# Performance work log

Measured on AMD Instinct MI355X. Metric: run time of the kernel, lower is better.

The kernel has to match this reference:

```python
import jax, jax.numpy as jnp
import numpy as np

B, N, DIN, DH, DOUT, E = 262144, 8, 3, 32, 1, 32


def setup_inputs() -> dict:
    key = jax.random.key(0)
    ks = jax.random.split(key, 8)
    x = jax.random.normal(ks[0], (B, N, DIN), dtype=jnp.float32)
    edge_index = jax.random.randint(ks[1], (2, E), 0, N, dtype=jnp.int64)
    s = lambda k, sh: jax.random.normal(k, sh, dtype=jnp.float32) * 0.1
    return {
        "x": x,
        "edge_index": edge_index,
        "W1": s(ks[2], (DIN, DH)),
        "b1": jnp.zeros((DH,), jnp.float32),
        "W2": s(ks[3], (DH, DH)),
        "b2": jnp.zeros((DH,), jnp.float32),
        "Wout": s(ks[4], (DH, DOUT)),
        "bout": jnp.zeros((DOUT,), jnp.float32),
    }


def _gcn_norm(edge_index, n):
    # add self loops, symmetric GCN normalization D^-1/2 (A+I) D^-1/2
    loops = jnp.arange(n, dtype=edge_index.dtype)
    src = jnp.concatenate([edge_index[0], loops])
    dst = jnp.concatenate([edge_index[1], loops])
    deg = jnp.zeros((n,), jnp.float32).at[dst].add(1.0)
    dinv = jax.lax.rsqrt(jnp.maximum(deg, 1e-12))
    norm = dinv[src] * dinv[dst]  # [E+N]
    return src, dst, norm


def _gcn_layer(h, W, b, src, dst, norm):
    hw = h @ W                              # [B, N, H]
    msg = hw[:, src, :] * norm[None, :, None]
    agg = jnp.zeros_like(hw).at[:, dst, :].add(msg)
    return agg + b


def reference(x, edge_index, W1, b1, W2, b2, Wout, bout):
    n = x.shape[1]
    src, dst, norm = _gcn_norm(edge_index, n)
    h = jax.nn.relu(_gcn_layer(x, W1, b1, src, dst, norm))
    h = jax.nn.relu(_gcn_layer(h, W2, b2, src, dst, norm))
    h = jax.nn.relu(h @ Wout + bout)        # [B, N, DOUT]
    # global_mean_pool with all-zero batch ids == mean over nodes
    return jnp.mean(h, axis=1)              # [B, DOUT]
```

## Files before the change

### kernel.cpp

```cpp
#include <hip/hip_runtime.h>


typedef __bf16 bf16x8 __attribute__((ext_vector_type(8)));
typedef float  f32x16 __attribute__((ext_vector_type(16)));

#define GPT 32

__global__ __launch_bounds__(256, 2) void gnn_kernel(
    const float* __restrict__ x,
    const int* __restrict__ ei,
    const float* __restrict__ W1,
    const float* __restrict__ b1,
    const float* __restrict__ W2,
    const float* __restrict__ b2,
    const float* __restrict__ Wout,
    const float* __restrict__ bout,
    float* __restrict__ out,
    int B, int ntiles)
{
    __shared__ float As[64];
    __shared__ float degs[8], dinvs[8];
    __shared__ float W1s[96], b1s[32], W2s[1024], b2s[32], Wouts[32];
    __shared__ float xs[2][GPT * 24];

    const int tid = threadIdx.x;

    if (tid < 96) W1s[tid] = W1[tid];
    if (tid < 64) As[tid] = 0.0f;
    if (tid < 32) { b1s[tid] = b1[tid]; b2s[tid] = b2[tid]; Wouts[tid] = Wout[tid]; }
    if (tid < 8)  degs[tid] = 1.0f;
    for (int i = tid; i < 1024; i += 256) W2s[i] = W2[i];
    __syncthreads();
    if (tid < 32) { int d = ei[32 + tid]; atomicAdd(&degs[d], 1.0f); }
    __syncthreads();
    if (tid < 8) dinvs[tid] = 1.0f / sqrtf(degs[tid]);
    __syncthreads();
    if (tid < 32) {
        int s = ei[tid], d = ei[32 + tid];
        atomicAdd(&As[d * 8 + s], dinvs[s] * dinvs[d]);
    } else if (tid < 40) {
        int n = tid - 32;
        atomicAdd(&As[n * 8 + n], dinvs[n] * dinvs[n]);
    }
    __syncthreads();

    const int lane = tid & 63;
    const int wv   = tid >> 6;
    const int r    = lane & 31;
    const int q    = lane >> 5;
    const int n8   = r & 7;
    const int gl   = r >> 3;
    const int g0   = wv * 4 + gl;
    const int g1   = 16 + wv * 4 + gl;

    float arow[8];
    #pragma unroll
    for (int m = 0; m < 8; m++) arow[m] = As[n8 * 8 + m];

    bf16x8 w1Ahi, w1Alo;
    #pragma unroll
    for (int j = 0; j < 8; j++) { w1Ahi[j] = (__bf16)0.0f; w1Alo[j] = (__bf16)0.0f; }
    #pragma unroll
    for (int j = 0; j < 3; j++) {
        float v = W1s[j * 32 + r];
        __bf16 h = (__bf16)v;
        w1Ahi[j] = h; w1Alo[j] = (__bf16)(v - (float)h);
    }
    {
        float v = b1s[r];
        __bf16 h = (__bf16)v;
        w1Ahi[3] = h; w1Alo[3] = (__bf16)(v - (float)h);
    }

    bf16x8 w2hi[2];
    #pragma unroll
    for (int s = 0; s < 2; s++) {
        #pragma unroll
        for (int j = 0; j < 8; j++) {
            int kk = 8 * s + j;
            int hid = (kk & 3) + 8 * (kk >> 2) + 4 * q;
            w2hi[s][j] = (__bf16)W2s[hid * 32 + r];
        }
    }
    bf16x8 a32hi[2];
    #pragma unroll
    for (int s = 0; s < 2; s++) {
        #pragma unroll
        for (int j = 0; j < 8; j++) {
            int kk = 8 * s + j;
            float v = ((kk >> 2) == gl) ? arow[(kk & 3) + 4 * q] : 0.0f;
            a32hi[s][j] = (__bf16)v;
        }
    }
    f32x16 zerov, b2rv;
    float woutr[16];
    #pragma unroll
    for (int k = 0; k < 16; k++) {
        int hk = (k & 3) + 8 * (k >> 2) + 4 * q;
        zerov[k] = 0.0f;
        b2rv[k] = b2s[hk];
        woutr[k] = Wouts[hk];
    }
    const float boutv = bout[0];

    const float4* x4 = reinterpret_cast<const float4*>(x);
    float4 nxt;
    if (tid < 192 && blockIdx.x < ntiles)
        nxt = x4[(long long)blockIdx.x * 192 + tid];
    int buf = 0;

    for (int tile = blockIdx.x; tile < ntiles; tile += gridDim.x) {
        const long long gbase = (long long)tile * GPT;
        if (tid < 192) *reinterpret_cast<float4*>(&xs[buf][tid * 4]) = nxt;
        __syncthreads();
        int tnext = tile + gridDim.x;
        if (tid < 192 && tnext < ntiles)
            nxt = x4[(long long)tnext * 192 + tid];

        float y00 = 0.f, y01 = 0.f, y02 = 0.f;
        {
            float xv[24];
            #pragma unroll
            for (int i = 0; i < 6; i++) {
                float4 v = *reinterpret_cast<float4*>(&xs[buf][g0 * 24 + i * 4]);
                xv[4 * i] = v.x; xv[4 * i + 1] = v.y; xv[4 * i + 2] = v.z; xv[4 * i + 3] = v.w;
            }
            #pragma unroll
            for (int m = 0; m < 8; m++) {
                y00 = fmaf(arow[m], xv[m * 3 + 0], y00);
                y01 = fmaf(arow[m], xv[m * 3 + 1], y01);
                y02 = fmaf(arow[m], xv[m * 3 + 2], y02);
            }
        }
        float y10 = 0.f, y11 = 0.f, y12 = 0.f;
        {
            float xv[24];
            #pragma unroll
            for (int i = 0; i < 6; i++) {
                float4 v = *reinterpret_cast<float4*>(&xs[buf][g1 * 24 + i * 4]);
                xv[4 * i] = v.x; xv[4 * i + 1] = v.y; xv[4 * i + 2] = v.z; xv[4 * i + 3] = v.w;
            }
            #pragma unroll
            for (int m = 0; m < 8; m++) {
                y10 = fmaf(arow[m], xv[m * 3 + 0], y10);
                y11 = fmaf(arow[m], xv[m * 3 + 1], y11);
                y12 = fmaf(arow[m], xv[m * 3 + 2], y12);
            }
        }

        bf16x8 yB0, yB1;
        #pragma unroll
        for (int j = 0; j < 8; j++) { yB0[j] = (__bf16)0.0f; yB1[j] = (__bf16)0.0f; }
        {
            __bf16 h0 = (__bf16)y00, h1 = (__bf16)y01, h2 = (__bf16)y02;
            yB0[0] = q ? (__bf16)(y00 - (float)h0) : h0;
            yB0[1] = q ? (__bf16)(y01 - (float)h1) : h1;
            yB0[2] = q ? (__bf16)(y02 - (float)h2) : h2;
            yB0[3] = q ? (__bf16)0.0f : (__bf16)1.0f;
            __bf16 g0h = (__bf16)y10, g1h = (__bf16)y11, g2h = (__bf16)y12;
            yB1[0] = q ? (__bf16)(y10 - (float)g0h) : g0h;
            yB1[1] = q ? (__bf16)(y11 - (float)g1h) : g1h;
            yB1[2] = q ? (__bf16)(y12 - (float)g2h) : g2h;
            yB1[3] = q ? (__bf16)0.0f : (__bf16)1.0f;
        }

        f32x16 vacc0, vacc1;
        vacc0 = __builtin_amdgcn_mfma_f32_32x32x16_bf16(w1Ahi, yB0, zerov, 0, 0, 0);
        vacc1 = __builtin_amdgcn_mfma_f32_32x32x16_bf16(w1Ahi, yB1, zerov, 0, 0, 0);
        vacc0 = __builtin_amdgcn_mfma_f32_32x32x16_bf16(w1Alo, yB0, vacc0, 0, 0, 0);
        vacc1 = __builtin_amdgcn_mfma_f32_32x32x16_bf16(w1Alo, yB1, vacc1, 0, 0, 0);

        bf16x8 phi0[2], phi1[2];
        #pragma unroll
        for (int s = 0; s < 2; s++) {
            #pragma unroll
            for (int j = 0; j < 8; j++) {
                phi0[s][j] = (__bf16)fmaxf(vacc0[8 * s + j], 0.0f);
                phi1[s][j] = (__bf16)fmaxf(vacc1[8 * s + j], 0.0f);
            }
        }

        vacc0 = __builtin_amdgcn_mfma_f32_32x32x16_bf16(phi0[0], w2hi[0], zerov, 0, 0, 0);
        vacc1 = __builtin_amdgcn_mfma_f32_32x32x16_bf16(phi1[0], w2hi[0], zerov, 0, 0, 0);
        vacc0 = __builtin_amdgcn_mfma_f32_32x32x16_bf16(phi0[1], w2hi[1], vacc0, 0, 0, 0);
        vacc1 = __builtin_amdgcn_mfma_f32_32x32x16_bf16(phi1[1], w2hi[1], vacc1, 0, 0, 0);

        bf16x8 thi0[2], thi1[2];
        #pragma unroll
        for (int s = 0; s < 2; s++) {
            #pragma unroll
            for (int j = 0; j < 8; j++) {
                thi0[s][j] = (__bf16)vacc0[8 * s + j];
                thi1[s][j] = (__bf16)vacc1[8 * s + j];
            }
        }

        vacc0 = __builtin_amdgcn_mfma_f32_32x32x16_bf16(thi0[0], a32hi[0], b2rv, 0, 0, 0);
        vacc1 = __builtin_amdgcn_mfma_f32_32x32x16_bf16(thi1[0], a32hi[0], b2rv, 0, 0, 0);
        vacc0 = __builtin_amdgcn_mfma_f32_32x32x16_bf16(thi0[1], a32hi[1], vacc0, 0, 0, 0);
        vacc1 = __builtin_amdgcn_mfma_f32_32x32x16_bf16(thi1[1], a32hi[1], vacc1, 0, 0, 0);

        float ss0 = 0.0f, ss1 = 0.0f;
        #pragma unroll
        for (int k = 0; k < 16; k++) {
            ss0 = fmaf(fmaxf(vacc0[k], 0.0f), woutr[k], ss0);
            ss1 = fmaf(fmaxf(vacc1[k], 0.0f), woutr[k], ss1);
        }
        ss0 += __shfl_xor(ss0, 32, 64);
        ss1 += __shfl_xor(ss1, 32, 64);
        float o0 = fmaxf(ss0 + boutv, 0.0f);
        float o1 = fmaxf(ss1 + boutv, 0.0f);
        o0 += __shfl_xor(o0, 1, 64);  o1 += __shfl_xor(o1, 1, 64);
        o0 += __shfl_xor(o0, 2, 64);  o1 += __shfl_xor(o1, 2, 64);
        o0 += __shfl_xor(o0, 4, 64);  o1 += __shfl_xor(o1, 4, 64);
        if (q == 0 && n8 == 0) {
            long long gg0 = gbase + g0;
            if (gg0 < (long long)B) out[gg0] = o0 * 0.125f;
            long long gg1 = gbase + g1;
            if (gg1 < (long long)B) out[gg1] = o1 * 0.125f;
        }
        buf ^= 1;
    }
}

extern "C" void kernel_launch(void* const* d_in, const int* in_sizes, int n_in,
                              void* d_out, int out_size, void* d_ws, size_t ws_size,
                              hipStream_t stream) {
    const float* x    = (const float*)d_in[0];
    const int*   ei   = (const int*)d_in[1];
    const float* W1   = (const float*)d_in[2];
    const float* b1   = (const float*)d_in[3];
    const float* W2   = (const float*)d_in[4];
    const float* b2   = (const float*)d_in[5];
    const float* Wout = (const float*)d_in[6];
    const float* bout = (const float*)d_in[7];
    float* out = (float*)d_out;
    (void)d_ws; (void)ws_size; (void)out_size; (void)n_in;

    const int B = in_sizes[0] / 24;
    const int ntiles = (B + GPT - 1) / GPT;
    const int grid = ntiles < 2048 ? ntiles : 2048;
    gnn_kernel<<<grid, 256, 0, stream>>>(x, ei, W1, b1, W2, b2, Wout, bout, out, B, ntiles);
}
```

Measured before the change: 32.34 us.

## Load each block's four tiles of x upfront instead of grid-stride double buffering

```diff
diff --git a/kernel.cpp b/kernel.cpp
--- a/kernel.cpp
+++ b/kernel.cpp
@@ -5,6 +5,7 @@
 typedef float  f32x16 __attribute__((ext_vector_type(16)));
 
 #define GPT 32
+#define TPB 4
 
 __global__ __launch_bounds__(256, 2) void gnn_kernel(
     const float* __restrict__ x,
@@ -16,12 +17,12 @@
     const float* __restrict__ Wout,
     const float* __restrict__ bout,
     float* __restrict__ out,
-    int B, int ntiles)
+    int B)
 {
     __shared__ float As[64];
     __shared__ float degs[8], dinvs[8];
     __shared__ float W1s[96], b1s[32], W2s[1024], b2s[32], Wouts[32];
-    __shared__ float xs[2][GPT * 24];
+    __shared__ float xs[TPB * GPT * 24];
 
     const int tid = threadIdx.x;
 
@@ -30,6 +31,14 @@
     if (tid < 32) { b1s[tid] = b1[tid]; b2s[tid] = b2[tid]; Wouts[tid] = Wout[tid]; }
     if (tid < 8)  degs[tid] = 1.0f;
     for (int i = tid; i < 1024; i += 256) W2s[i] = W2[i];
+    {
+        const float4* x4 = reinterpret_cast<const float4*>(x);
+        long long base4 = (long long)blockIdx.x * (TPB * GPT * 6);
+        float4* xs4 = reinterpret_cast<float4*>(xs);
+        #pragma unroll
+        for (int i = 0; i < 3; i++)
+            xs4[tid + 256 * i] = x4[base4 + tid + 256 * i];
+    }
     __syncthreads();
     if (tid < 32) { int d = ei[32 + tid]; atomicAdd(&degs[d], 1.0f); }
     __syncthreads();
@@ -103,26 +112,17 @@
     }
     const float boutv = bout[0];
 
-    const float4* x4 = reinterpret_cast<const float4*>(x);
-    float4 nxt;
-    if (tid < 192 && blockIdx.x < ntiles)
-        nxt = x4[(long long)blockIdx.x * 192 + tid];
-    int buf = 0;
-
-    for (int tile = blockIdx.x; tile < ntiles; tile += gridDim.x) {
-        const long long gbase = (long long)tile * GPT;
-        if (tid < 192) *reinterpret_cast<float4*>(&xs[buf][tid * 4]) = nxt;
-        __syncthreads();
-        int tnext = tile + gridDim.x;
-        if (tid < 192 && tnext < ntiles)
-            nxt = x4[(long long)tnext * 192 + tid];
+    #pragma unroll
+    for (int it = 0; it < TPB; it++) {
+        const long long gbase = ((long long)blockIdx.x * TPB + it) * GPT;
+        const float* xt = &xs[it * GPT * 24];
 
         float y00 = 0.f, y01 = 0.f, y02 = 0.f;
         {
             float xv[24];
             #pragma unroll
             for (int i = 0; i < 6; i++) {
-                float4 v = *reinterpret_cast<float4*>(&xs[buf][g0 * 24 + i * 4]);
+                float4 v = *reinterpret_cast<const float4*>(&xt[g0 * 24 + i * 4]);
                 xv[4 * i] = v.x; xv[4 * i + 1] = v.y; xv[4 * i + 2] = v.z; xv[4 * i + 3] = v.w;
             }
             #pragma unroll
@@ -137,7 +137,7 @@
             float xv[24];
             #pragma unroll
             for (int i = 0; i < 6; i++) {
-                float4 v = *reinterpret_cast<float4*>(&xs[buf][g1 * 24 + i * 4]);
+                float4 v = *reinterpret_cast<const float4*>(&xt[g1 * 24 + i * 4]);
                 xv[4 * i] = v.x; xv[4 * i + 1] = v.y; xv[4 * i + 2] = v.z; xv[4 * i + 3] = v.w;
             }
             #pragma unroll
@@ -219,7 +219,6 @@
             long long gg1 = gbase + g1;
             if (gg1 < (long long)B) out[gg1] = o1 * 0.125f;
         }
-        buf ^= 1;
     }
 }
 
@@ -238,7 +237,6 @@
     (void)d_ws; (void)ws_size; (void)out_size; (void)n_in;
 
     const int B = in_sizes[0] / 24;
-    const int ntiles = (B + GPT - 1) / GPT;
-    const int grid = ntiles < 2048 ? ntiles : 2048;
-    gnn_kernel<<<grid, 256, 0, stream>>>(x, ei, W1, b1, W2, b2, Wout, bout, out, B, ntiles);
+    const int grid = B / (TPB * GPT);
+    gnn_kernel<<<grid, 256, 0, stream>>>(x, ei, W1, b1, W2, b2, Wout, bout, out, B);
 }
```

New measurement: 31.53 us. 2.5% less time.
